# Performance work log

Measured on AMD Instinct MI355X. Metric: run time of the kernel, lower is better.

Reference implementation:

```python
import jax, jax.numpy as jnp
import numpy as np

N_NODES = 50000
N_EDGES = 800000
IN_DIM = 64
OUT_DIM = 64
HID = OUT_DIM // 2  # 32
N_LAYERS = 9  # layer_num; layer_num >= 7 => no temporal conv, conv dropout unused


def _layernorm(x, w, b, eps=1e-5):
    mu = jnp.mean(x, axis=-1, keepdims=True)
    var = jnp.var(x, axis=-1, keepdims=True)
    return (x - mu) * jax.lax.rsqrt(var + eps) * w + b


def _conv(x, Wp, Wn, Ws, src, tgt, pos_m, neg_m):
    # relation-wise gather -> linear -> masked merge -> single scatter_add
    xs = x[src]  # [E, d_in]
    m = jnp.where(pos_m[:, None], xs @ Wp.T, 0.0) + jnp.where(neg_m[:, None], xs @ Wn.T, 0.0)
    agg = jax.ops.segment_sum(m, tgt, num_segments=N_NODES)
    return agg + x @ Ws.T


def _asfr(x, ln_w, ln_b, gw, gb):
    xn = _layernorm(x, ln_w, ln_b)
    w = jax.nn.sigmoid(xn @ gw.T + gb)
    w1 = jnp.where(w > 0.5, 1.0, w)
    w2 = jnp.where(w > 0.5, 0.0, w)
    x1 = w1 * x
    x2 = w2 * x
    h = x.shape[1] // 2
    return jnp.concatenate([x1[:, :h] + x2[:, h:], x1[:, h:] + x2[:, :h]], axis=1)


def setup_inputs() -> dict:
    key = jax.random.key(0)
    ks = jax.random.split(key, 24)
    init_emb = jax.random.normal(ks[0], (N_NODES, IN_DIM), dtype=jnp.float32)
    src = jax.random.randint(ks[1], (N_EDGES,), 0, N_NODES)
    tgt = jax.random.randint(ks[2], (N_EDGES,), 0, N_NODES)
    sign = jnp.where(jax.random.uniform(ks[3], (N_EDGES,)) > 0.5, 1, -1).astype(jnp.int64)
    edge_index_s = jnp.stack([src, tgt, sign], axis=1).astype(jnp.int64)

    def w(k, shape, fan_in):
        return jax.random.normal(k, shape, dtype=jnp.float32) * (1.0 / np.sqrt(fan_in))

    inp = dict(init_emb=init_emb, edge_index_s=edge_index_s)
    # conv1: in 64 -> 32, relations pos/neg + self loop (no bias)
    inp["W1_pos"] = w(ks[4], (HID, IN_DIM), IN_DIM)
    inp["W1_neg"] = w(ks[5], (HID, IN_DIM), IN_DIM)
    inp["W1_self"] = w(ks[6], (HID, IN_DIM), IN_DIM)
    # 8 further convs: 32 -> 32, stacked
    L = N_LAYERS - 1
    inp["Wl_pos"] = w(ks[7], (L, HID, HID), HID)
    inp["Wl_neg"] = w(ks[8], (L, HID, HID), HID)
    inp["Wl_self"] = w(ks[9], (L, HID, HID), HID)
    # ASFR
    inp["asfr_ln_w"] = jnp.ones((HID,), jnp.float32)
    inp["asfr_ln_b"] = jnp.zeros((HID,), jnp.float32)
    inp["asfr_gate_w"] = w(ks[10], (HID, HID), HID)
    inp["asfr_gate_b"] = jnp.zeros((HID,), jnp.float32)
    # projection 32 -> 64
    inp["proj_w"] = w(ks[11], (OUT_DIM, HID), HID)
    inp["proj_b"] = jnp.zeros((OUT_DIM,), jnp.float32)
    # readout MLP: 64 -> 64 -> 64 -> 1, layernorm + relu between
    inp["mlp_w1"] = w(ks[12], (OUT_DIM, OUT_DIM), OUT_DIM)
    inp["mlp_b1"] = jnp.zeros((OUT_DIM,), jnp.float32)
    inp["mlp_ln1_w"] = jnp.ones((OUT_DIM,), jnp.float32)
    inp["mlp_ln1_b"] = jnp.zeros((OUT_DIM,), jnp.float32)
    inp["mlp_w2"] = w(ks[13], (OUT_DIM, OUT_DIM), OUT_DIM)
    inp["mlp_b2"] = jnp.zeros((OUT_DIM,), jnp.float32)
    inp["mlp_ln2_w"] = jnp.ones((OUT_DIM,), jnp.float32)
    inp["mlp_ln2_b"] = jnp.zeros((OUT_DIM,), jnp.float32)
    inp["mlp_w3"] = w(ks[14], (1, OUT_DIM), OUT_DIM)
    inp["mlp_b3"] = jnp.zeros((1,), jnp.float32)
    return inp


def reference(init_emb, edge_index_s, W1_pos, W1_neg, W1_self, Wl_pos, Wl_neg, Wl_self,
              asfr_ln_w, asfr_ln_b, asfr_gate_w, asfr_gate_b, proj_w, proj_b,
              mlp_w1, mlp_b1, mlp_ln1_w, mlp_ln1_b, mlp_w2, mlp_b2,
              mlp_ln2_w, mlp_ln2_b, mlp_w3, mlp_b3):
    src = edge_index_s[:, 0]
    tgt = edge_index_s[:, 1]
    sign = edge_index_s[:, 2]
    pos_m = sign > 0
    neg_m = sign < 0

    z = jax.nn.elu(_conv(init_emb, W1_pos, W1_neg, W1_self, src, tgt, pos_m, neg_m))
    z = _asfr(z, asfr_ln_w, asfr_ln_b, asfr_gate_w, asfr_gate_b)
    for i in range(Wl_pos.shape[0]):
        z_new = jax.nn.elu(_conv(z, Wl_pos[i], Wl_neg[i], Wl_self[i], src, tgt, pos_m, neg_m))
        z = z_new if i == 0 else z_new + 0.1 * z
    z = jax.nn.elu(z @ proj_w.T + proj_b)
    # readout MLP (eval mode: dropout identity)
    h = jax.nn.relu(_layernorm(z @ mlp_w1.T + mlp_b1, mlp_ln1_w, mlp_ln1_b))
    h = jax.nn.relu(_layernorm(h @ mlp_w2.T + mlp_b2, mlp_ln2_w, mlp_ln2_b))
    prob = jax.nn.sigmoid(h @ mlp_w3.T + mlp_b3)
    return (z, prob)
```

## Files before the change

### kernel.cpp

```cpp
#include <hip/hip_runtime.h>
#include <hip/hip_bf16.h>

#define NODES 50000
#define EDGES 800000
#define BSH 8
#define NBUCK 196
#define NBIN_BLOCKS 391

__device__ __forceinline__ float elu1(float x) { return x > 0.f ? x : expm1f(x); }

union F4 { float4 v; float f[4]; };

__global__ __launch_bounds__(256) void k_hist2(const int* __restrict__ ei, int* __restrict__ deg,
                                               int* __restrict__ bucket_cnt) {
  __shared__ int cnt[NBUCK];
  int t = threadIdx.x;
  for (int i = t; i < NBUCK; i += 256) cnt[i] = 0;
  __syncthreads();
  int base = blockIdx.x * 2048;
#pragma unroll
  for (int i = 0; i < 8; i++) {
    int e = base + i * 256 + t;
    if (e < EDGES) {
      int tgt = ei[e * 3 + 1];
      atomicAdd(deg + tgt, 1);
      atomicAdd(&cnt[tgt >> BSH], 1);
    }
  }
  __syncthreads();
  for (int i = t; i < NBUCK; i += 256)
    if (cnt[i]) atomicAdd(bucket_cnt + i, cnt[i]);
}

__global__ __launch_bounds__(512) void k_scan1(const int* __restrict__ deg, int* __restrict__ offs,
                                               int* __restrict__ bsum) {
  __shared__ int s[512];
  int t = threadIdx.x, i = blockIdx.x * 512 + t;
  int v = (i < NODES) ? deg[i] : 0;
  s[t] = v;
  __syncthreads();
  for (int o = 1; o < 512; o <<= 1) {
    int x = (t >= o) ? s[t - o] : 0;
    __syncthreads();
    s[t] += x;
    __syncthreads();
  }
  if (i < NODES) offs[i] = s[t] - v;
  if (t == 511) bsum[blockIdx.x] = s[511];
}

__global__ __launch_bounds__(128) void k_scan2(int* __restrict__ bsum, int nb) {
  __shared__ int s[128];
  int t = threadIdx.x;
  int v = (t < nb) ? bsum[t] : 0;
  s[t] = v;
  __syncthreads();
  for (int o = 1; o < 128; o <<= 1) {
    int x = (t >= o) ? s[t - o] : 0;
    __syncthreads();
    s[t] += x;
    __syncthreads();
  }
  if (t < nb) bsum[t] = s[t] - v;
}

__global__ __launch_bounds__(512) void k_scan3(int* __restrict__ offs, const int* __restrict__ bsum) {
  int i = blockIdx.x * 512 + threadIdx.x;
  if (i < NODES) offs[i] += bsum[blockIdx.x];
  if (i == 0) offs[NODES] = EDGES;
}

__global__ __launch_bounds__(256) void k_bscan(const int* __restrict__ bucket_cnt,
                                               int* __restrict__ bucket_base,
                                               int* __restrict__ bucket_cursor) {
  __shared__ int s[256];
  int t = threadIdx.x;
  int v = (t < NBUCK) ? bucket_cnt[t] : 0;
  s[t] = v;
  __syncthreads();
  for (int o = 1; o < 256; o <<= 1) {
    int x = (t >= o) ? s[t - o] : 0;
    __syncthreads();
    s[t] += x;
    __syncthreads();
  }
  if (t < NBUCK) { int e = s[t] - v; bucket_base[t] = e; bucket_cursor[t] = e; }
}

__global__ __launch_bounds__(256) void k_bin(const int* __restrict__ ei,
                                             int* __restrict__ bucket_cursor,
                                             unsigned* __restrict__ binned) {
  __shared__ int cnt[NBUCK], base[NBUCK];
  int t = threadIdx.x;
  for (int i = t; i < NBUCK; i += 256) cnt[i] = 0;
  __syncthreads();
  int eb = blockIdx.x * 2048;
#pragma unroll
  for (int i = 0; i < 8; i++) {
    int e = eb + i * 256 + t;
    if (e < EDGES) atomicAdd(&cnt[ei[e * 3 + 1] >> BSH], 1);
  }
  __syncthreads();
  for (int i = t; i < NBUCK; i += 256) {
    int c = cnt[i];
    base[i] = c ? atomicAdd(bucket_cursor + i, c) : 0;
    cnt[i] = 0;
  }
  __syncthreads();
#pragma unroll
  for (int i = 0; i < 8; i++) {
    int e = eb + i * 256 + t;
    if (e < EDGES) {
      int src = ei[e * 3 + 0];
      int tgt = ei[e * 3 + 1];
      int sg  = ei[e * 3 + 2];
      unsigned val = (unsigned)src | (sg < 0 ? 0x10000u : 0u) | ((unsigned)(tgt & 255) << 17);
      int bkt = tgt >> BSH;
      int r = atomicAdd(&cnt[bkt], 1);
      binned[base[bkt] + r] = val;
    }
  }
}

__global__ __launch_bounds__(256) void k_scatter2(const unsigned* __restrict__ binned,
                                                  const int* __restrict__ bucket_base,
                                                  const int* __restrict__ bucket_cnt,
                                                  const int* __restrict__ offs,
                                                  unsigned* __restrict__ perm) {
  __shared__ int cur[256];
  int b = blockIdx.x, t = threadIdx.x;
  int t0 = b << BSH;
  cur[t] = (t0 + t < NODES) ? offs[t0 + t] : 0;
  __syncthreads();
  int n = bucket_cnt[b], bb = bucket_base[b];
  for (int i = t; i < n; i += 256) {
    unsigned e = binned[bb + i];
    int p = atomicAdd(&cur[(e >> 17) & 255], 1);
    perm[p] = (e & 0xFFFFu) | ((e & 0x10000u) << 15);
  }
}

__global__ __launch_bounds__(256) void k_lin64(const float* __restrict__ x,
    const float* __restrict__ Wp, const float* __restrict__ Wn, const float* __restrict__ Ws,
    __hip_bfloat16* __restrict__ ypb, __hip_bfloat16* __restrict__ ynb, float* __restrict__ ys) {
  constexpr int K4 = 16;
  __shared__ float4 wp[K4][32], wn[K4][32], wsm[K4][32];
  __shared__ float4 xs[8][K4];
  for (int i = threadIdx.x; i < 32 * K4; i += 256) {
    int k4 = i >> 5, c = i & 31;
    wp[k4][c]  = ((const float4*)Wp)[c * K4 + k4];
    wn[k4][c]  = ((const float4*)Wn)[c * K4 + k4];
    wsm[k4][c] = ((const float4*)Ws)[c * K4 + k4];
  }
  int base = blockIdx.x * 8;
  for (int i = threadIdx.x; i < 8 * K4; i += 256) {
    int r = i / K4, k4 = i - r * K4;
    xs[r][k4] = ((const float4*)(x + (size_t)(base + r) * 64))[k4];
  }
  __syncthreads();
  int lane = threadIdx.x & 31, local = threadIdx.x >> 5;
  float ap = 0.f, an = 0.f, asf = 0.f;
#pragma unroll
  for (int k4 = 0; k4 < K4; k4++) {
    float4 xv = xs[local][k4];
    float4 a = wp[k4][lane], b = wn[k4][lane], c = wsm[k4][lane];
    ap  = fmaf(xv.w, a.w, fmaf(xv.z, a.z, fmaf(xv.y, a.y, fmaf(xv.x, a.x, ap))));
    an  = fmaf(xv.w, b.w, fmaf(xv.z, b.z, fmaf(xv.y, b.y, fmaf(xv.x, b.x, an))));
    asf = fmaf(xv.w, c.w, fmaf(xv.z, c.z, fmaf(xv.y, c.y, fmaf(xv.x, c.x, asf))));
  }
  size_t o = (size_t)(base + local) * 32 + lane;
  ypb[o] = __float2bfloat16(ap);
  ynb[o] = __float2bfloat16(an);
  ys[o] = asf;
}

#define ACC8(A, V)                                   \
  A[0] += __uint_as_float((V).x << 16);              \
  A[1] += __uint_as_float((V).x & 0xffff0000u);      \
  A[2] += __uint_as_float((V).y << 16);              \
  A[3] += __uint_as_float((V).y & 0xffff0000u);      \
  A[4] += __uint_as_float((V).z << 16);              \
  A[5] += __uint_as_float((V).z & 0xffff0000u);      \
  A[6] += __uint_as_float((V).w << 16);              \
  A[7] += __uint_as_float((V).w & 0xffff0000u);

template <int DO_ASFR, int DO_RES, int DO_LIN, int WRITE_Z>
__global__ __launch_bounds__(256) void k_layer(
    const unsigned short* __restrict__ ypi, const unsigned short* __restrict__ yni,
    float* __restrict__ ys,
    const unsigned* __restrict__ perm, const int* __restrict__ offs,
    float* __restrict__ z,
    const float* __restrict__ lnw, const float* __restrict__ lnb,
    const float* __restrict__ gw, const float* __restrict__ gb,
    const float* __restrict__ Wp, const float* __restrict__ Wn, const float* __restrict__ Ws,
    __hip_bfloat16* __restrict__ ypo, __hip_bfloat16* __restrict__ yno) {
  __shared__ float4 wps[8][32], wns[8][32], wss[8][32], gws[8][32];
  __shared__ float zrow[8][36], xrow[8][36];
  int t = threadIdx.x;
  if (DO_LIN) {
    int k4 = t >> 5, c = t & 31;
    wps[k4][c] = ((const float4*)Wp)[c * 8 + k4];
    wns[k4][c] = ((const float4*)Wn)[c * 8 + k4];
    wss[k4][c] = ((const float4*)Ws)[c * 8 + k4];
    if (DO_ASFR) gws[k4][c] = ((const float4*)gw)[c * 8 + k4];
  }
  int lane = t & 31, local = t >> 5;
  int node = blockIdx.x * 8 + local;
  int es = lane >> 2, fs = lane & 3;
  int beg = offs[node], end = offs[node + 1];
  float a0[8], a1[8], a2[8], a3[8];
#pragma unroll
  for (int i = 0; i < 8; i++) { a0[i] = 0.f; a1[i] = 0.f; a2[i] = 0.f; a3[i] = 0.f; }
  for (int base = beg; base < end; base += 32) {
    unsigned pe = (base + lane < end) ? perm[base + lane] : 0u;
    int rem = end - base;
    unsigned u0 = __shfl(pe, es, 32);
    unsigned u1 = __shfl(pe, es + 8, 32);
    const unsigned short* p0 = (u0 >> 31) ? yni : ypi;
    const unsigned short* p1 = (u1 >> 31) ? yni : ypi;
    uint4 v0 = *((const uint4*)(p0 + (size_t)(u0 & 0x7FFFFFFFu) * 32) + fs);
    uint4 v1 = *((const uint4*)(p1 + (size_t)(u1 & 0x7FFFFFFFu) * 32) + fs);
    if (es < rem) { ACC8(a0, v0); }
    if (es + 8 < rem) { ACC8(a1, v1); }
    if (rem > 16) {
      unsigned u2 = __shfl(pe, es + 16, 32);
      unsigned u3 = __shfl(pe, es + 24, 32);
      const unsigned short* p2 = (u2 >> 31) ? yni : ypi;
      const unsigned short* p3 = (u3 >> 31) ? yni : ypi;
      uint4 v2 = *((const uint4*)(p2 + (size_t)(u2 & 0x7FFFFFFFu) * 32) + fs);
      uint4 v3 = *((const uint4*)(p3 + (size_t)(u3 & 0x7FFFFFFFu) * 32) + fs);
      if (es + 16 < rem) { ACC8(a2, v2); }
      if (es + 24 < rem) { ACC8(a3, v3); }
    }
  }
#pragma unroll
  for (int i = 0; i < 8; i++) a0[i] += (a1[i] + a2[i]) + a3[i];
#pragma unroll
  for (int m = 4; m <= 16; m <<= 1) {
#pragma unroll
    for (int i = 0; i < 8; i++) a0[i] += __shfl_xor(a0[i], m, 32);
  }
  if (es == 0) {
    const float* ysr = ys + (size_t)node * 32 + fs * 8;
    F4 s0, s1;
    s0.v = *(const float4*)ysr;
    s1.v = *(const float4*)(ysr + 4);
    float o[8];
#pragma unroll
    for (int i = 0; i < 4; i++) o[i] = elu1(a0[i] + s0.f[i]);
#pragma unroll
    for (int i = 0; i < 4; i++) o[4 + i] = elu1(a0[4 + i] + s1.f[i]);
    if (DO_RES) {
      const float* rr = z + (size_t)node * 32 + fs * 8;
      F4 r0, r1;
      r0.v = *(const float4*)rr;
      r1.v = *(const float4*)(rr + 4);
#pragma unroll
      for (int i = 0; i < 4; i++) { o[i] += 0.1f * r0.f[i]; o[4 + i] += 0.1f * r1.f[i]; }
    }
#pragma unroll
    for (int i = 0; i < 8; i++) zrow[local][fs * 8 + i] = o[i];
    if (WRITE_Z) {
      float* zw = z + (size_t)node * 32 + fs * 8;
      *(float4*)zw = make_float4(o[0], o[1], o[2], o[3]);
      *(float4*)(zw + 4) = make_float4(o[4], o[5], o[6], o[7]);
    }
  }
  __syncthreads();
  if (!DO_LIN) return;
  if (DO_ASFR) {
    float v = zrow[local][lane];
    float s = v;
#pragma unroll
    for (int m = 16; m; m >>= 1) s += __shfl_xor(s, m, 32);
    float mu = s * (1.f / 32.f);
    float d = v - mu, sq = d * d;
#pragma unroll
    for (int m = 16; m; m >>= 1) sq += __shfl_xor(sq, m, 32);
    float xn = d * rsqrtf(sq * (1.f / 32.f) + 1e-5f) * lnw[lane] + lnb[lane];
    xrow[local][lane] = xn;
    float ga = gb[lane];
#pragma unroll
    for (int k4 = 0; k4 < 8; k4++) {
      float4 xv = *((const float4*)&xrow[local][0] + k4);
      float4 w = gws[k4][lane];
      ga = fmaf(xv.w, w.w, fmaf(xv.z, w.z, fmaf(xv.y, w.y, fmaf(xv.x, w.x, ga))));
    }
    float g = 1.f / (1.f + __expf(-ga));
    float w1 = g > 0.5f ? 1.f : g;
    float w2 = g > 0.5f ? 0.f : g;
    float zn = w1 * v + __shfl_xor(w2 * v, 16, 32);
    zrow[local][lane] = zn;
  }
  float ap = 0.f, an = 0.f, asf = 0.f;
#pragma unroll
  for (int k4 = 0; k4 < 8; k4++) {
    float4 xv = *((const float4*)&zrow[local][0] + k4);
    float4 a2w = wps[k4][lane], b2 = wns[k4][lane], c2 = wss[k4][lane];
    ap  = fmaf(xv.w, a2w.w, fmaf(xv.z, a2w.z, fmaf(xv.y, a2w.y, fmaf(xv.x, a2w.x, ap))));
    an  = fmaf(xv.w, b2.w, fmaf(xv.z, b2.z, fmaf(xv.y, b2.y, fmaf(xv.x, b2.x, an))));
    asf = fmaf(xv.w, c2.w, fmaf(xv.z, c2.z, fmaf(xv.y, c2.y, fmaf(xv.x, c2.x, asf))));
  }
  size_t o = (size_t)node * 32 + lane;
  ypo[o] = __float2bfloat16(ap);
  yno[o] = __float2bfloat16(an);
  ys[o] = asf;
}

__global__ __launch_bounds__(256) void k_mlp(const float* __restrict__ z,
    const float* __restrict__ pw, const float* __restrict__ pb,
    const float* __restrict__ w1, const float* __restrict__ b1,
    const float* __restrict__ l1w, const float* __restrict__ l1b,
    const float* __restrict__ w2, const float* __restrict__ b2,
    const float* __restrict__ l2w, const float* __restrict__ l2b,
    const float* __restrict__ w3, const float* __restrict__ b3,
    float* __restrict__ outz, float* __restrict__ outp) {
  __shared__ float4 wbuf[1536];
  __shared__ float4 hbuf4[128 * 17];
  __shared__ float pb_s[64], b1_s[64], l1w_s[64], l1b_s[64], b2_s[64], l2w_s[64], l2b_s[64], w3_s[64];
  int t = threadIdx.x;
  for (int i = t; i < 512; i += 256) {
    int k = i >> 4, j4 = i & 15;
    float4 v;
    v.x = pw[(j4 * 4 + 0) * 32 + k]; v.y = pw[(j4 * 4 + 1) * 32 + k];
    v.z = pw[(j4 * 4 + 2) * 32 + k]; v.w = pw[(j4 * 4 + 3) * 32 + k];
    wbuf[i] = v;
  }
  for (int i = t; i < 1024; i += 256) {
    int k = i >> 4, j4 = i & 15;
    float4 v;
    v.x = w1[(j4 * 4 + 0) * 64 + k]; v.y = w1[(j4 * 4 + 1) * 64 + k];
    v.z = w1[(j4 * 4 + 2) * 64 + k]; v.w = w1[(j4 * 4 + 3) * 64 + k];
    wbuf[512 + i] = v;
  }
  if (t < 64) {
    pb_s[t] = pb[t]; b1_s[t] = b1[t]; l1w_s[t] = l1w[t]; l1b_s[t] = l1b[t];
    b2_s[t] = b2[t]; l2w_s[t] = l2w[t]; l2b_s[t] = l2b[t]; w3_s[t] = w3[t];
  }
  __syncthreads();
  int g = t >> 3, q = t & 7;
  int nb0 = blockIdx.x * 128 + g;
  float bb3 = b3[0];
  bool live[4];
#pragma unroll
  for (int n = 0; n < 4; n++) live[n] = (nb0 + 32 * n) < NODES;
  float acc[4][8], h[4][8];
#pragma unroll
  for (int n = 0; n < 4; n++)
    if (live[n])
      hbuf4[(n * 32 + g) * 17 + q] = ((const float4*)(z + (size_t)(nb0 + 32 * n) * 32))[q];
#pragma unroll
  for (int n = 0; n < 4; n++)
#pragma unroll
    for (int i = 0; i < 8; i++) acc[n][i] = pb_s[q * 8 + i];
#pragma unroll 2
  for (int k4 = 0; k4 < 8; k4++) {
    F4 hv[4];
#pragma unroll
    for (int n = 0; n < 4; n++) hv[n].v = hbuf4[(n * 32 + g) * 17 + k4];
#pragma unroll
    for (int c = 0; c < 4; c++) {
      float4 wa = wbuf[(k4 * 4 + c) * 16 + q * 2];
      float4 wb = wbuf[(k4 * 4 + c) * 16 + q * 2 + 1];
#pragma unroll
      for (int n = 0; n < 4; n++) {
        float hk = hv[n].f[c];
        acc[n][0] = fmaf(hk, wa.x, acc[n][0]); acc[n][1] = fmaf(hk, wa.y, acc[n][1]);
        acc[n][2] = fmaf(hk, wa.z, acc[n][2]); acc[n][3] = fmaf(hk, wa.w, acc[n][3]);
        acc[n][4] = fmaf(hk, wb.x, acc[n][4]); acc[n][5] = fmaf(hk, wb.y, acc[n][5]);
        acc[n][6] = fmaf(hk, wb.z, acc[n][6]); acc[n][7] = fmaf(hk, wb.w, acc[n][7]);
      }
    }
  }
#pragma unroll
  for (int n = 0; n < 4; n++) {
#pragma unroll
    for (int i = 0; i < 8; i++) h[n][i] = elu1(acc[n][i]);
    float4 h0 = make_float4(h[n][0], h[n][1], h[n][2], h[n][3]);
    float4 h1 = make_float4(h[n][4], h[n][5], h[n][6], h[n][7]);
    if (live[n]) {
      float4* oz = (float4*)(outz + (size_t)(nb0 + 32 * n) * 64 + q * 8);
      oz[0] = h0; oz[1] = h1;
    }
    hbuf4[(n * 32 + g) * 17 + 2 * q] = h0;
    hbuf4[(n * 32 + g) * 17 + 2 * q + 1] = h1;
  }
#pragma unroll
  for (int n = 0; n < 4; n++)
#pragma unroll
    for (int i = 0; i < 8; i++) acc[n][i] = b1_s[q * 8 + i];
#pragma unroll 2
  for (int k4 = 0; k4 < 16; k4++) {
    F4 hv[4];
#pragma unroll
    for (int n = 0; n < 4; n++) hv[n].v = hbuf4[(n * 32 + g) * 17 + k4];
#pragma unroll
    for (int c = 0; c < 4; c++) {
      float4 wa = wbuf[512 + (k4 * 4 + c) * 16 + q * 2];
      float4 wb = wbuf[512 + (k4 * 4 + c) * 16 + q * 2 + 1];
#pragma unroll
      for (int n = 0; n < 4; n++) {
        float hk = hv[n].f[c];
        acc[n][0] = fmaf(hk, wa.x, acc[n][0]); acc[n][1] = fmaf(hk, wa.y, acc[n][1]);
        acc[n][2] = fmaf(hk, wa.z, acc[n][2]); acc[n][3] = fmaf(hk, wa.w, acc[n][3]);
        acc[n][4] = fmaf(hk, wb.x, acc[n][4]); acc[n][5] = fmaf(hk, wb.y, acc[n][5]);
        acc[n][6] = fmaf(hk, wb.z, acc[n][6]); acc[n][7] = fmaf(hk, wb.w, acc[n][7]);
      }
    }
  }
  __syncthreads();
  for (int i = t; i < 1024; i += 256) {
    int k = i >> 4, j4 = i & 15;
    float4 v;
    v.x = w2[(j4 * 4 + 0) * 64 + k]; v.y = w2[(j4 * 4 + 1) * 64 + k];
    v.z = w2[(j4 * 4 + 2) * 64 + k]; v.w = w2[(j4 * 4 + 3) * 64 + k];
    wbuf[i] = v;
  }
#pragma unroll
  for (int n = 0; n < 4; n++) {
    float s = 0.f;
#pragma unroll
    for (int i = 0; i < 8; i++) s += acc[n][i];
    s += __shfl_xor(s, 1, 8); s += __shfl_xor(s, 2, 8); s += __shfl_xor(s, 4, 8);
    float mu = s * (1.f / 64.f);
    float vs = 0.f;
#pragma unroll
    for (int i = 0; i < 8; i++) { float dd = acc[n][i] - mu; vs += dd * dd; }
    vs += __shfl_xor(vs, 1, 8); vs += __shfl_xor(vs, 2, 8); vs += __shfl_xor(vs, 4, 8);
    float rs = rsqrtf(vs * (1.f / 64.f) + 1e-5f);
#pragma unroll
    for (int i = 0; i < 8; i++)
      h[n][i] = fmaxf((acc[n][i] - mu) * rs * l1w_s[q * 8 + i] + l1b_s[q * 8 + i], 0.f);
  }
  __syncthreads();
#pragma unroll
  for (int n = 0; n < 4; n++) {
    hbuf4[(n * 32 + g) * 17 + 2 * q] = make_float4(h[n][0], h[n][1], h[n][2], h[n][3]);
    hbuf4[(n * 32 + g) * 17 + 2 * q + 1] = make_float4(h[n][4], h[n][5], h[n][6], h[n][7]);
  }
#pragma unroll
  for (int n = 0; n < 4; n++)
#pragma unroll
    for (int i = 0; i < 8; i++) acc[n][i] = b2_s[q * 8 + i];
#pragma unroll 2
  for (int k4 = 0; k4 < 16; k4++) {
    F4 hv[4];
#pragma unroll
    for (int n = 0; n < 4; n++) hv[n].v = hbuf4[(n * 32 + g) * 17 + k4];
#pragma unroll
    for (int c = 0; c < 4; c++) {
      float4 wa = wbuf[(k4 * 4 + c) * 16 + q * 2];
      float4 wb = wbuf[(k4 * 4 + c) * 16 + q * 2 + 1];
#pragma unroll
      for (int n = 0; n < 4; n++) {
        float hk = hv[n].f[c];
        acc[n][0] = fmaf(hk, wa.x, acc[n][0]); acc[n][1] = fmaf(hk, wa.y, acc[n][1]);
        acc[n][2] = fmaf(hk, wa.z, acc[n][2]); acc[n][3] = fmaf(hk, wa.w, acc[n][3]);
        acc[n][4] = fmaf(hk, wb.x, acc[n][4]); acc[n][5] = fmaf(hk, wb.y, acc[n][5]);
        acc[n][6] = fmaf(hk, wb.z, acc[n][6]); acc[n][7] = fmaf(hk, wb.w, acc[n][7]);
      }
    }
  }
#pragma unroll
  for (int n = 0; n < 4; n++) {
    float s = 0.f;
#pragma unroll
    for (int i = 0; i < 8; i++) s += acc[n][i];
    s += __shfl_xor(s, 1, 8); s += __shfl_xor(s, 2, 8); s += __shfl_xor(s, 4, 8);
    float mu = s * (1.f / 64.f);
    float vs = 0.f;
#pragma unroll
    for (int i = 0; i < 8; i++) { float dd = acc[n][i] - mu; vs += dd * dd; }
    vs += __shfl_xor(vs, 1, 8); vs += __shfl_xor(vs, 2, 8); vs += __shfl_xor(vs, 4, 8);
    float rs = rsqrtf(vs * (1.f / 64.f) + 1e-5f);
    float p = 0.f;
#pragma unroll
    for (int i = 0; i < 8; i++) {
      float hv2 = fmaxf((acc[n][i] - mu) * rs * l2w_s[q * 8 + i] + l2b_s[q * 8 + i], 0.f);
      p = fmaf(hv2, w3_s[q * 8 + i], p);
    }
    p += __shfl_xor(p, 1, 8); p += __shfl_xor(p, 2, 8); p += __shfl_xor(p, 4, 8);
    if (q == 0 && live[n]) outp[nb0 + 32 * n] = 1.f / (1.f + __expf(-(p + bb3)));
  }
}

extern "C" void kernel_launch(void* const* d_in, const int* in_sizes, int n_in,
                              void* d_out, int out_size, void* d_ws, size_t ws_size,
                              hipStream_t stream) {
  const float* init_emb = (const float*)d_in[0];
  const int*   ei  = (const int*)d_in[1];
  const float* W1p = (const float*)d_in[2];
  const float* W1n = (const float*)d_in[3];
  const float* W1s = (const float*)d_in[4];
  const float* Wlp = (const float*)d_in[5];
  const float* Wln = (const float*)d_in[6];
  const float* Wls = (const float*)d_in[7];
  const float* lnw = (const float*)d_in[8];
  const float* lnb = (const float*)d_in[9];
  const float* gw  = (const float*)d_in[10];
  const float* gb  = (const float*)d_in[11];
  const float* pw  = (const float*)d_in[12];
  const float* pb  = (const float*)d_in[13];
  const float* w1  = (const float*)d_in[14];
  const float* b1  = (const float*)d_in[15];
  const float* l1w = (const float*)d_in[16];
  const float* l1b = (const float*)d_in[17];
  const float* w2  = (const float*)d_in[18];
  const float* b2  = (const float*)d_in[19];
  const float* l2w = (const float*)d_in[20];
  const float* l2b = (const float*)d_in[21];
  const float* w3  = (const float*)d_in[22];
  const float* b3  = (const float*)d_in[23];

  char* ws = (char*)d_ws;
  size_t off = 0;
  auto alloc = [&](size_t b) { void* p = ws + off; off = (off + b + 255) & ~(size_t)255; return p; };
  __hip_bfloat16* ypA = (__hip_bfloat16*)alloc(NODES * 32 * 2);
  __hip_bfloat16* ynA = (__hip_bfloat16*)alloc(NODES * 32 * 2);
  __hip_bfloat16* ypB = (__hip_bfloat16*)alloc(NODES * 32 * 2);
  __hip_bfloat16* ynB = (__hip_bfloat16*)alloc(NODES * 32 * 2);
  float*    ysel   = (float*)alloc(NODES * 32 * 4);
  float*    zbuf   = (float*)alloc(NODES * 32 * 4);
  unsigned* perm   = (unsigned*)alloc(EDGES * 4);
  int*      deg    = (int*)alloc(NODES * 4);
  int*      offs   = (int*)alloc((NODES + 1) * 4);
  int*      bsum   = (int*)alloc(128 * 4);
  int*      bucket_cnt    = (int*)alloc(NBUCK * 4);
  int*      bucket_base   = (int*)alloc(NBUCK * 4);
  int*      bucket_cursor = (int*)alloc(NBUCK * 4);
  unsigned* binned = (unsigned*)ypA;

  hipMemsetAsync(deg, 0, NODES * 4, stream);
  hipMemsetAsync(bucket_cnt, 0, NBUCK * 4, stream);
  k_hist2<<<NBIN_BLOCKS, 256, 0, stream>>>(ei, deg, bucket_cnt);
  int nb = (NODES + 511) / 512;
  k_scan1<<<nb, 512, 0, stream>>>(deg, offs, bsum);
  k_scan2<<<1, 128, 0, stream>>>(bsum, nb);
  k_scan3<<<nb, 512, 0, stream>>>(offs, bsum);
  k_bscan<<<1, 256, 0, stream>>>(bucket_cnt, bucket_base, bucket_cursor);
  k_bin<<<NBIN_BLOCKS, 256, 0, stream>>>(ei, bucket_cursor, binned);
  k_scatter2<<<NBUCK, 256, 0, stream>>>(binned, bucket_base, bucket_cnt, offs, perm);

  const int G = NODES / 8;
  k_lin64<<<G, 256, 0, stream>>>(init_emb, W1p, W1n, W1s, ypA, ynA, ysel);
  k_layer<1, 0, 1, 0><<<G, 256, 0, stream>>>((const unsigned short*)ypA, (const unsigned short*)ynA,
      ysel, perm, offs, zbuf, lnw, lnb, gw, gb, Wlp, Wln, Wls, ypB, ynB);
  k_layer<0, 0, 1, 1><<<G, 256, 0, stream>>>((const unsigned short*)ypB, (const unsigned short*)ynB,
      ysel, perm, offs, zbuf, nullptr, nullptr, nullptr, nullptr,
      Wlp + 1024, Wln + 1024, Wls + 1024, ypA, ynA);
  const __hip_bfloat16* yin_p = ypA; const __hip_bfloat16* yin_n = ynA;
  __hip_bfloat16* yout_p = ypB; __hip_bfloat16* yout_n = ynB;
  for (int i = 1; i < 7; i++) {
    k_layer<0, 1, 1, 1><<<G, 256, 0, stream>>>((const unsigned short*)yin_p, (const unsigned short*)yin_n,
        ysel, perm, offs, zbuf, nullptr, nullptr, nullptr, nullptr,
        Wlp + (i + 1) * 1024, Wln + (i + 1) * 1024, Wls + (i + 1) * 1024, yout_p, yout_n);
    const __hip_bfloat16* tp = yin_p; const __hip_bfloat16* tn = yin_n;
    yin_p = yout_p; yin_n = yout_n;
    yout_p = (__hip_bfloat16*)tp; yout_n = (__hip_bfloat16*)tn;
  }
  k_layer<0, 1, 0, 1><<<G, 256, 0, stream>>>((const unsigned short*)yin_p, (const unsigned short*)yin_n,
      ysel, perm, offs, zbuf, nullptr, nullptr, nullptr, nullptr,
      nullptr, nullptr, nullptr, nullptr, nullptr);

  float* outz = (float*)d_out;
  float* outp = outz + (size_t)NODES * 64;
  k_mlp<<<(NODES + 127) / 128, 256, 0, stream>>>(zbuf, pw, pb, w1, b1, l1w, l1b,
                                                 w2, b2, l2w, l2b, w3, b3, outz, outp);
}
```

Before: 381.0 us.

## Derive CSR offsets from per-bucket local histograms instead of global degree scan

Removes the global per-node degree histogram (800k global atomics), its memset, and the three-kernel prefix scan. Each bucket block in the scatter kernel now counts its 256 targets in shared memory, scans them locally, and writes node offsets relative to the bucket base. This drops four launches and the global atomic traffic, at the cost of one extra read pass over the binned edges inside the scatter kernel.

Result: faster. 347.2 us (-8.9%).

```diff
diff --git a/kernel.cpp b/kernel.cpp
--- a/kernel.cpp
+++ b/kernel.cpp
@@ -11,8 +11,7 @@
 
 union F4 { float4 v; float f[4]; };
 
-__global__ __launch_bounds__(256) void k_hist2(const int* __restrict__ ei, int* __restrict__ deg,
-                                               int* __restrict__ bucket_cnt) {
+__global__ __launch_bounds__(256) void k_bhist(const int* __restrict__ ei, int* __restrict__ bucket_cnt) {
   __shared__ int cnt[NBUCK];
   int t = threadIdx.x;
   for (int i = t; i < NBUCK; i += 256) cnt[i] = 0;
@@ -21,53 +20,11 @@
 #pragma unroll
   for (int i = 0; i < 8; i++) {
     int e = base + i * 256 + t;
-    if (e < EDGES) {
-      int tgt = ei[e * 3 + 1];
-      atomicAdd(deg + tgt, 1);
-      atomicAdd(&cnt[tgt >> BSH], 1);
-    }
+    if (e < EDGES) atomicAdd(&cnt[ei[e * 3 + 1] >> BSH], 1);
   }
   __syncthreads();
   for (int i = t; i < NBUCK; i += 256)
     if (cnt[i]) atomicAdd(bucket_cnt + i, cnt[i]);
-}
-
-__global__ __launch_bounds__(512) void k_scan1(const int* __restrict__ deg, int* __restrict__ offs,
-                                               int* __restrict__ bsum) {
-  __shared__ int s[512];
-  int t = threadIdx.x, i = blockIdx.x * 512 + t;
-  int v = (i < NODES) ? deg[i] : 0;
-  s[t] = v;
-  __syncthreads();
-  for (int o = 1; o < 512; o <<= 1) {
-    int x = (t >= o) ? s[t - o] : 0;
-    __syncthreads();
-    s[t] += x;
-    __syncthreads();
-  }
-  if (i < NODES) offs[i] = s[t] - v;
-  if (t == 511) bsum[blockIdx.x] = s[511];
-}
-
-__global__ __launch_bounds__(128) void k_scan2(int* __restrict__ bsum, int nb) {
-  __shared__ int s[128];
-  int t = threadIdx.x;
-  int v = (t < nb) ? bsum[t] : 0;
-  s[t] = v;
-  __syncthreads();
-  for (int o = 1; o < 128; o <<= 1) {
-    int x = (t >= o) ? s[t - o] : 0;
-    __syncthreads();
-    s[t] += x;
-    __syncthreads();
-  }
-  if (t < nb) bsum[t] = s[t] - v;
-}
-
-__global__ __launch_bounds__(512) void k_scan3(int* __restrict__ offs, const int* __restrict__ bsum) {
-  int i = blockIdx.x * 512 + threadIdx.x;
-  if (i < NODES) offs[i] += bsum[blockIdx.x];
-  if (i == 0) offs[NODES] = EDGES;
 }
 
 __global__ __launch_bounds__(256) void k_bscan(const int* __restrict__ bucket_cnt,
@@ -90,7 +47,7 @@
 __global__ __launch_bounds__(256) void k_bin(const int* __restrict__ ei,
                                              int* __restrict__ bucket_cursor,
                                              unsigned* __restrict__ binned) {
-  __shared__ int cnt[NBUCK], base[NBUCK];
+  __shared__ int cnt[NBUCK], basec[NBUCK];
   int t = threadIdx.x;
   for (int i = t; i < NBUCK; i += 256) cnt[i] = 0;
   __syncthreads();
@@ -103,7 +60,7 @@
   __syncthreads();
   for (int i = t; i < NBUCK; i += 256) {
     int c = cnt[i];
-    base[i] = c ? atomicAdd(bucket_cursor + i, c) : 0;
+    basec[i] = c ? atomicAdd(bucket_cursor + i, c) : 0;
     cnt[i] = 0;
   }
   __syncthreads();
@@ -117,7 +74,7 @@
       unsigned val = (unsigned)src | (sg < 0 ? 0x10000u : 0u) | ((unsigned)(tgt & 255) << 17);
       int bkt = tgt >> BSH;
       int r = atomicAdd(&cnt[bkt], 1);
-      binned[base[bkt] + r] = val;
+      binned[basec[bkt] + r] = val;
     }
   }
 }
@@ -125,17 +82,34 @@
 __global__ __launch_bounds__(256) void k_scatter2(const unsigned* __restrict__ binned,
                                                   const int* __restrict__ bucket_base,
                                                   const int* __restrict__ bucket_cnt,
-                                                  const int* __restrict__ offs,
+                                                  int* __restrict__ offs,
                                                   unsigned* __restrict__ perm) {
-  __shared__ int cur[256];
+  __shared__ int cnt[256];
+  __shared__ int s[256];
   int b = blockIdx.x, t = threadIdx.x;
   int t0 = b << BSH;
-  cur[t] = (t0 + t < NODES) ? offs[t0 + t] : 0;
+  cnt[t] = 0;
   __syncthreads();
   int n = bucket_cnt[b], bb = bucket_base[b];
+  for (int i = t; i < n; i += 256) atomicAdd(&cnt[(binned[bb + i] >> 17) & 255], 1);
+  __syncthreads();
+  int v = cnt[t];
+  s[t] = v;
+  __syncthreads();
+  for (int o = 1; o < 256; o <<= 1) {
+    int x = (t >= o) ? s[t - o] : 0;
+    __syncthreads();
+    s[t] += x;
+    __syncthreads();
+  }
+  int pos = bb + s[t] - v;
+  if (t0 + t < NODES) offs[t0 + t] = pos;
+  cnt[t] = pos;
+  if (b == 0 && t == 0) offs[NODES] = EDGES;
+  __syncthreads();
   for (int i = t; i < n; i += 256) {
     unsigned e = binned[bb + i];
-    int p = atomicAdd(&cur[(e >> 17) & 255], 1);
+    int p = atomicAdd(&cnt[(e >> 17) & 255], 1);
     perm[p] = (e & 0xFFFFu) | ((e & 0x10000u) << 15);
   }
 }
@@ -522,21 +496,14 @@
   float*    ysel   = (float*)alloc(NODES * 32 * 4);
   float*    zbuf   = (float*)alloc(NODES * 32 * 4);
   unsigned* perm   = (unsigned*)alloc(EDGES * 4);
-  int*      deg    = (int*)alloc(NODES * 4);
   int*      offs   = (int*)alloc((NODES + 1) * 4);
-  int*      bsum   = (int*)alloc(128 * 4);
   int*      bucket_cnt    = (int*)alloc(NBUCK * 4);
   int*      bucket_base   = (int*)alloc(NBUCK * 4);
   int*      bucket_cursor = (int*)alloc(NBUCK * 4);
   unsigned* binned = (unsigned*)ypA;
 
-  hipMemsetAsync(deg, 0, NODES * 4, stream);
   hipMemsetAsync(bucket_cnt, 0, NBUCK * 4, stream);
-  k_hist2<<<NBIN_BLOCKS, 256, 0, stream>>>(ei, deg, bucket_cnt);
-  int nb = (NODES + 511) / 512;
-  k_scan1<<<nb, 512, 0, stream>>>(deg, offs, bsum);
-  k_scan2<<<1, 128, 0, stream>>>(bsum, nb);
-  k_scan3<<<nb, 512, 0, stream>>>(offs, bsum);
+  k_bhist<<<NBIN_BLOCKS, 256, 0, stream>>>(ei, bucket_cnt);
   k_bscan<<<1, 256, 0, stream>>>(bucket_cnt, bucket_base, bucket_cursor);
   k_bin<<<NBIN_BLOCKS, 256, 0, stream>>>(ei, bucket_cursor, binned);
   k_scatter2<<<NBUCK, 256, 0, stream>>>(binned, bucket_base, bucket_cnt, offs, perm);
```
